# Kernel tuning notes

Measured on AMD Instinct MI355X. Metric: run time of the kernel, lower is better.

## Reference

```python
import jax, jax.numpy as jnp
import numpy as np

N_NODES = 100000
N_EDGES = 1600000
DIM = 128


def setup_inputs() -> dict:
    key = jax.random.key(0)
    k1, k2, k3, k4, k5 = jax.random.split(key, 5)
    x = jax.random.normal(k1, (N_NODES, DIM), dtype=jnp.float32)
    edge_index = jax.random.randint(k2, (2, N_EDGES), 0, N_NODES, dtype=jnp.int64)
    s = 1.0 / np.sqrt(DIM)
    W_lin = jax.random.uniform(k3, (DIM, DIM), jnp.float32, -s, s)   # nn.Linear (bias=False)
    W_gcn = jax.random.uniform(k4, (DIM, DIM), jnp.float32, -s, s)   # GCNConv internal lin (bias=False)
    b_gcn = jax.random.uniform(k5, (DIM,), jnp.float32, -s, s)       # GCNConv bias
    return {"x": x, "edge_index": edge_index, "W_lin": W_lin, "W_gcn": W_gcn, "b_gcn": b_gcn}


def reference(x, edge_index, W_lin, W_gcn, b_gcn):
    N = x.shape[0]
    # self.linear (bias=False) then GCNConv's internal linear (bias=False)
    h = (x @ W_lin.T) @ W_gcn.T                                      # [N, D]
    # add self loops (PyG GCNConv default add_self_loops=True)
    loop = jnp.arange(N, dtype=edge_index.dtype)
    row = jnp.concatenate([edge_index[0], loop])                     # source
    col = jnp.concatenate([edge_index[1], loop])                     # target
    # symmetric normalization: deg over targets incl. self loops
    deg = jax.ops.segment_sum(jnp.ones_like(col, dtype=h.dtype), col, num_segments=N)
    dinv = jnp.where(deg > 0, jax.lax.rsqrt(deg), 0.0)               # deg^{-1/2}, inf->0
    norm = dinv[row] * dinv[col]                                     # [E+N]
    # gather -> scale -> scatter-add (aggr='add', flow source_to_target)
    msg = h[row] * norm[:, None]                                     # [E+N, D]
    out = jax.ops.segment_sum(msg, col, num_segments=N) + b_gcn      # [N, D]
    # NOTE: self.relu is `Sequential as ReLU` -> empty Sequential -> identity
    return out
```

## Files before the change

kernel.cpp:

```cpp
#include <hip/hip_runtime.h>
#include <hip/hip_bf16.h>

#define DIM 128
#define NBUCK 2048
#define BCAP 1344
#define NPART 256

typedef short bf16x8 __attribute__((ext_vector_type(8)));
typedef float f32x4 __attribute__((ext_vector_type(4)));

__device__ __forceinline__ unsigned short f2bf(float f) {
    __hip_bfloat16 h = __float2bfloat16(f);
    return *reinterpret_cast<unsigned short*>(&h);
}
__device__ __forceinline__ float u2f(unsigned int u) {
    union { unsigned int i; float f; } v; v.i = u; return v.f;
}
__device__ __forceinline__ unsigned int f2u(float f) {
    union { float f; unsigned int i; } v; v.f = f; return v.i;
}

__global__ __launch_bounds__(256) void part_wp_kernel(
        const int* __restrict__ src, const int* __restrict__ dst,
        int* __restrict__ bcur, unsigned int* __restrict__ ebuf,
        int E, int nchunk,
        const float* __restrict__ Wg, const float* __restrict__ Wl,
        unsigned short* __restrict__ Wpb) {
    __shared__ int hist[NBUCK];
    __shared__ int base[NBUCK];
    const int t = threadIdx.x;

    if (blockIdx.x >= NPART) {
        const int id = (blockIdx.x - NPART) * 256 + t;
        const int c = id >> 7, k = id & 127;
        float s = 0.f;
        for (int j = 0; j < DIM; ++j)
            s = fmaf(Wg[c * DIM + j], Wl[j * DIM + k], s);
        Wpb[c * DIM + k] = f2bf(s);
        return;
    }

    for (int i = t; i < NBUCK; i += 256) hist[i] = 0;
    __syncthreads();

    const int e0 = blockIdx.x * nchunk;
    const int e1 = min(e0 + nchunk, E);
    for (int e = e0 + t; e < e1; e += 256)
        atomicAdd(&hist[dst[e] >> 6], 1);
    __syncthreads();

    for (int i = t; i < NBUCK; i += 256) {
        const int cc = hist[i];
        base[i] = (cc > 0) ? atomicAdd(&bcur[i], cc) : 0;
    }
    __syncthreads();

    for (int e = e0 + t; e < e1; e += 256) {
        const int d = dst[e];
        const int b = d >> 6;
        const int pos = atomicAdd(&base[b], 1);
        if (pos < BCAP)
            ebuf[(size_t)b * BCAP + pos] =
                (unsigned int)src[e] | ((unsigned int)(d & 63) << 17);
    }
}

__global__ __launch_bounds__(256) void gemm_bcount_kernel(
        const float* __restrict__ x, const unsigned short* __restrict__ Wpb,
        unsigned int* __restrict__ hbu,
        const unsigned int* __restrict__ ebuf, const int* __restrict__ bcur,
        int* __restrict__ degi, float* __restrict__ dinv,
        int N, int ntile) {
    __shared__ __align__(16) char smem[49152];
    const int t = threadIdx.x;

    if (blockIdx.x >= ntile) {
        int* cnt = (int*)smem;
        const int bkt = blockIdx.x - ntile;
        if (t < 64) cnt[t] = 0;
        __syncthreads();
        const int c = min(bcur[bkt], BCAP);
        const unsigned int* eb = ebuf + (size_t)bkt * BCAP;
        for (int i = t; i < c; i += 256)
            atomicAdd(&cnt[eb[i] >> 17], 1);
        __syncthreads();
        if (t < 64) {
            const int node = (bkt << 6) + t;
            if (node < N) {
                degi[node] = cnt[t];
                dinv[node] = rsqrtf((float)(cnt[t] + 1));
            }
        }
        return;
    }

    unsigned short* xs  = (unsigned short*)smem;
    unsigned short* wps = xs + 64 * 128;
    const int brow = blockIdx.x * 64;

#pragma unroll
    for (int j = 0; j < 8; ++j) {
        const int col = (t >> 4) + j * 16;
        const int kb = t & 15;
        const uint4 v = *(const uint4*)(Wpb + col * 128 + kb * 8);
        *(uint4*)&wps[col * 128 + ((kb ^ (col & 15)) * 8)] = v;
    }
#pragma unroll
    for (int i = 0; i < 4; ++i) {
        const int row = (t >> 4) + i * 16;
        const int kb = t & 15;
        const int g = brow + row;
        float4 a0 = make_float4(0.f, 0.f, 0.f, 0.f), a1 = a0;
        if (g < N) {
            a0 = *(const float4*)(x + (size_t)g * 128 + kb * 8);
            a1 = *(const float4*)(x + (size_t)g * 128 + kb * 8 + 4);
        }
        ushort4 lo, hi;
        lo.x = f2bf(a0.x); lo.y = f2bf(a0.y); lo.z = f2bf(a0.z); lo.w = f2bf(a0.w);
        hi.x = f2bf(a1.x); hi.y = f2bf(a1.y); hi.z = f2bf(a1.z); hi.w = f2bf(a1.w);
        unsigned short* p = &xs[row * 128 + ((kb ^ (row & 15)) * 8)];
        *(ushort4*)p = lo;
        *(ushort4*)(p + 4) = hi;
    }
    __syncthreads();

    const int lane = t & 63, wv = t >> 6;
    const int m16 = lane & 15, quad = lane >> 4;

    f32x4 acc[8];
#pragma unroll
    for (int ct = 0; ct < 8; ++ct) acc[ct] = (f32x4){0.f, 0.f, 0.f, 0.f};

    const int arow = wv * 16 + m16;
#pragma unroll
    for (int s = 0; s < 4; ++s) {
        const int pk = ((s * 4 + quad) ^ m16) * 8;
        const bf16x8 a = *(const bf16x8*)&xs[arow * 128 + pk];
#pragma unroll
        for (int ct = 0; ct < 8; ++ct) {
            const bf16x8 b = *(const bf16x8*)&wps[(ct * 16 + m16) * 128 + pk];
            acc[ct] = __builtin_amdgcn_mfma_f32_16x16x32_bf16(a, b, acc[ct], 0, 0, 0);
        }
    }

    const int r0 = brow + wv * 16 + quad * 4;
#pragma unroll
    for (int ct = 0; ct < 4; ++ct) {
        const int col = ct * 16 + m16;
#pragma unroll
        for (int r = 0; r < 4; ++r) {
            if (r0 + r < N) {
                const unsigned int pk = (unsigned int)f2bf(acc[ct][r]) |
                                        ((unsigned int)f2bf(acc[ct + 4][r]) << 16);
                hbu[(size_t)(r0 + r) * 64 + col] = pk;
            }
        }
    }
}

__global__ __launch_bounds__(256) void sortgather_kernel(
        const unsigned int* __restrict__ hbu, const unsigned int* __restrict__ ebuf,
        const int* __restrict__ bcur, const int* __restrict__ degi,
        const float* __restrict__ dinv,
        const float* __restrict__ b, float* __restrict__ out, int N) {
    __shared__ unsigned int pairs[BCAP * 2];
    __shared__ int cnt[64];
    __shared__ int scn[64];
    __shared__ int st[64];
    __shared__ int deg[64];
    const int t   = threadIdx.x;
    const int bkt = blockIdx.x;
    const int c   = min(bcur[bkt], BCAP);
    const unsigned int* eb = ebuf + (size_t)bkt * BCAP;
    const int n0 = bkt << 6;

    if (t < 64) {
        const int node = n0 + t;
        const int d = (node < N) ? degi[node] : 0;
        deg[t] = d;
        scn[t] = d;
    }
    __syncthreads();
    for (int off = 1; off < 64; off <<= 1) {
        int v = (t < 64 && t >= off) ? scn[t - off] : 0;
        __syncthreads();
        if (t < 64) scn[t] += v;
        __syncthreads();
    }
    if (t < 64) {
        const int excl = scn[t] - deg[t];
        st[t]  = excl;
        cnt[t] = excl;
    }
    __syncthreads();

    for (int i = t; i < c; i += 256) {
        const unsigned int p = eb[i];
        const int s = (int)(p & 0x1FFFF);
        const int pos = atomicAdd(&cnt[p >> 17], 1);
        uint2 pr; pr.x = (unsigned int)s; pr.y = f2u(dinv[s]);
        *(uint2*)&pairs[2 * pos] = pr;
    }
    __syncthreads();

    const int lane = t & 63;
    const int wv   = t >> 6;
    const float bx = b[lane];
    const float by = b[lane + 64];

    for (int i = 0; i < 16; ++i) {
        const int dl = wv * 16 + i;
        const int node = n0 + dl;
        if (node >= N) continue;
        const int dgi = deg[dl];
        const float dv = rsqrtf((float)(dgi + 1));
        const unsigned int self = hbu[(size_t)node * 64 + lane];
        float ax = dv * u2f(self << 16);
        float ay = dv * u2f(self & 0xFFFF0000u);

        const int jb = st[dl];
        const int je = jb + dgi;
        int j = jb;
        for (; j + 8 <= je; j += 8) {
            const uint2 p0 = *(const uint2*)&pairs[2 * (j + 0)];
            const uint2 p1 = *(const uint2*)&pairs[2 * (j + 1)];
            const uint2 p2 = *(const uint2*)&pairs[2 * (j + 2)];
            const uint2 p3 = *(const uint2*)&pairs[2 * (j + 3)];
            const uint2 p4 = *(const uint2*)&pairs[2 * (j + 4)];
            const uint2 p5 = *(const uint2*)&pairs[2 * (j + 5)];
            const uint2 p6 = *(const uint2*)&pairs[2 * (j + 6)];
            const uint2 p7 = *(const uint2*)&pairs[2 * (j + 7)];
            const unsigned int v0 = hbu[(size_t)p0.x * 64 + lane];
            const unsigned int v1 = hbu[(size_t)p1.x * 64 + lane];
            const unsigned int v2 = hbu[(size_t)p2.x * 64 + lane];
            const unsigned int v3 = hbu[(size_t)p3.x * 64 + lane];
            const unsigned int v4 = hbu[(size_t)p4.x * 64 + lane];
            const unsigned int v5 = hbu[(size_t)p5.x * 64 + lane];
            const unsigned int v6 = hbu[(size_t)p6.x * 64 + lane];
            const unsigned int v7 = hbu[(size_t)p7.x * 64 + lane];
            ax = fmaf(u2f(v0 << 16), u2f(p0.y), ax);
            ax = fmaf(u2f(v1 << 16), u2f(p1.y), ax);
            ax = fmaf(u2f(v2 << 16), u2f(p2.y), ax);
            ax = fmaf(u2f(v3 << 16), u2f(p3.y), ax);
            ax = fmaf(u2f(v4 << 16), u2f(p4.y), ax);
            ax = fmaf(u2f(v5 << 16), u2f(p5.y), ax);
            ax = fmaf(u2f(v6 << 16), u2f(p6.y), ax);
            ax = fmaf(u2f(v7 << 16), u2f(p7.y), ax);
            ay = fmaf(u2f(v0 & 0xFFFF0000u), u2f(p0.y), ay);
            ay = fmaf(u2f(v1 & 0xFFFF0000u), u2f(p1.y), ay);
            ay = fmaf(u2f(v2 & 0xFFFF0000u), u2f(p2.y), ay);
            ay = fmaf(u2f(v3 & 0xFFFF0000u), u2f(p3.y), ay);
            ay = fmaf(u2f(v4 & 0xFFFF0000u), u2f(p4.y), ay);
            ay = fmaf(u2f(v5 & 0xFFFF0000u), u2f(p5.y), ay);
            ay = fmaf(u2f(v6 & 0xFFFF0000u), u2f(p6.y), ay);
            ay = fmaf(u2f(v7 & 0xFFFF0000u), u2f(p7.y), ay);
        }
        for (; j + 2 <= je; j += 2) {
            const uint2 p0 = *(const uint2*)&pairs[2 * (j + 0)];
            const uint2 p1 = *(const uint2*)&pairs[2 * (j + 1)];
            const unsigned int v0 = hbu[(size_t)p0.x * 64 + lane];
            const unsigned int v1 = hbu[(size_t)p1.x * 64 + lane];
            ax = fmaf(u2f(v0 << 16), u2f(p0.y), ax);
            ax = fmaf(u2f(v1 << 16), u2f(p1.y), ax);
            ay = fmaf(u2f(v0 & 0xFFFF0000u), u2f(p0.y), ay);
            ay = fmaf(u2f(v1 & 0xFFFF0000u), u2f(p1.y), ay);
        }
        for (; j < je; ++j) {
            const uint2 pr = *(const uint2*)&pairs[2 * j];
            const unsigned int v = hbu[(size_t)pr.x * 64 + lane];
            ax = fmaf(u2f(v << 16), u2f(pr.y), ax);
            ay = fmaf(u2f(v & 0xFFFF0000u), u2f(pr.y), ay);
        }
        out[(size_t)node * 128 + lane]      = dv * ax + bx;
        out[(size_t)node * 128 + 64 + lane] = dv * ay + by;
    }
}

extern "C" void kernel_launch(void* const* d_in, const int* in_sizes, int n_in,
                              void* d_out, int out_size, void* d_ws, size_t ws_size,
                              hipStream_t stream) {
    const float* x  = (const float*)d_in[0];
    const int*   ei = (const int*)d_in[1];
    const float* Wl = (const float*)d_in[2];
    const float* Wg = (const float*)d_in[3];
    const float* bg = (const float*)d_in[4];

    const int N = in_sizes[0] / DIM;
    const int E = in_sizes[1] / 2;
    const int* srcIdx = ei;
    const int* dstIdx = ei + E;

    char* wsb = (char*)d_ws;
    unsigned short* Wpb  = (unsigned short*)(wsb + 0);
    int*            bcur = (int*)(wsb + 65536);
    int*            degi = (int*)(wsb + 131072);
    float*          dinv = (float*)(wsb + 589824);
    unsigned int*   ebuf = (unsigned int*)(wsb + 2097152);
    unsigned int*   hbu  = (unsigned int*)(wsb + 16777216);
    const size_t needed = 16777216ull + (size_t)N * DIM * 2;
    if (ws_size < needed) return;

    const int nbkt  = (N + 63) >> 6;
    const int ntile = (N + 63) >> 6;
    const int nchunk = (E + NPART - 1) / NPART;

    hipMemsetAsync(bcur, 0, NBUCK * sizeof(int), stream);
    part_wp_kernel    <<<NPART + 64, 256, 0, stream>>>(srcIdx, dstIdx, bcur, ebuf,
                                                       E, nchunk, Wg, Wl, Wpb);
    gemm_bcount_kernel<<<ntile + nbkt, 256, 0, stream>>>(x, Wpb, hbu, ebuf, bcur,
                                                         degi, dinv, N, ntile);
    sortgather_kernel <<<nbkt, 256, 0, stream>>>(hbu, ebuf, bcur, degi, dinv, bg,
                                                 (float*)d_out, N);
}
```

Baseline: 218.5 us.

## Partition edges into per-block bucket slots and split gather into half-buckets

The edge partition no longer uses global atomics to reserve bucket space. Each of 48 large blocks writes into its own fixed-capacity slot per bucket and records per-slot counts, with a global overflow list for slots that fill up. The gather kernel now runs two blocks per 64-node bucket, each taking 32 nodes, which doubles the block count and halves shared memory per block. In exchange every half-block scans the whole bucket's slots and the overflow list, so it reads the edge data twice and does more filtering work.

```diff
diff --git a/kernel.cpp b/kernel.cpp
--- a/kernel.cpp
+++ b/kernel.cpp
@@ -3,8 +3,10 @@
 
 #define DIM 128
 #define NBUCK 2048
-#define BCAP 1344
-#define NPART 256
+#define PBLK 48
+#define CAPPB 52
+#define OVFCAP 4096
+#define HCAP 896
 
 typedef short bf16x8 __attribute__((ext_vector_type(8)));
 typedef float f32x4 __attribute__((ext_vector_type(4)));
@@ -20,18 +22,17 @@
     union { float f; unsigned int i; } v; v.f = f; return v.i;
 }
 
-__global__ __launch_bounds__(256) void part_wp_kernel(
+__global__ __launch_bounds__(1024) void part_wp_kernel(
         const int* __restrict__ src, const int* __restrict__ dst,
-        int* __restrict__ bcur, unsigned int* __restrict__ ebuf,
+        unsigned int* __restrict__ ebuf, int* __restrict__ cntt,
+        int* __restrict__ ovf_cnt, uint2* __restrict__ ovf,
         int E, int nchunk,
         const float* __restrict__ Wg, const float* __restrict__ Wl,
         unsigned short* __restrict__ Wpb) {
-    __shared__ int hist[NBUCK];
-    __shared__ int base[NBUCK];
     const int t = threadIdx.x;
 
-    if (blockIdx.x >= NPART) {
-        const int id = (blockIdx.x - NPART) * 256 + t;
+    if (blockIdx.x >= PBLK) {
+        const int id = (blockIdx.x - PBLK) * 1024 + t;
         const int c = id >> 7, k = id & 127;
         float s = 0.f;
         for (int j = 0; j < DIM; ++j)
@@ -40,35 +41,41 @@
         return;
     }
 
-    for (int i = t; i < NBUCK; i += 256) hist[i] = 0;
-    __syncthreads();
-
-    const int e0 = blockIdx.x * nchunk;
+    __shared__ int hist[NBUCK];
+    const int blk = blockIdx.x;
+    for (int i = t; i < NBUCK; i += 1024) hist[i] = 0;
+    __syncthreads();
+
+    const int e0 = blk * nchunk;
     const int e1 = min(e0 + nchunk, E);
-    for (int e = e0 + t; e < e1; e += 256)
+    for (int e = e0 + t; e < e1; e += 1024)
         atomicAdd(&hist[dst[e] >> 6], 1);
     __syncthreads();
 
-    for (int i = t; i < NBUCK; i += 256) {
-        const int cc = hist[i];
-        base[i] = (cc > 0) ? atomicAdd(&bcur[i], cc) : 0;
-    }
-    __syncthreads();
-
-    for (int e = e0 + t; e < e1; e += 256) {
+    for (int i = t; i < NBUCK; i += 1024) cntt[i * PBLK + blk] = hist[i];
+    __syncthreads();
+    for (int i = t; i < NBUCK; i += 1024) hist[i] = 0;
+    __syncthreads();
+
+    for (int e = e0 + t; e < e1; e += 1024) {
         const int d = dst[e];
         const int b = d >> 6;
-        const int pos = atomicAdd(&base[b], 1);
-        if (pos < BCAP)
-            ebuf[(size_t)b * BCAP + pos] =
+        const int pos = atomicAdd(&hist[b], 1);
+        if (pos < CAPPB) {
+            ebuf[((size_t)b * PBLK + blk) * CAPPB + pos] =
                 (unsigned int)src[e] | ((unsigned int)(d & 63) << 17);
+        } else {
+            const int op = atomicAdd(ovf_cnt, 1);
+            if (op < OVFCAP) { uint2 o; o.x = (unsigned int)src[e]; o.y = (unsigned int)d; ovf[op] = o; }
+        }
     }
 }
 
 __global__ __launch_bounds__(256) void gemm_bcount_kernel(
         const float* __restrict__ x, const unsigned short* __restrict__ Wpb,
         unsigned int* __restrict__ hbu,
-        const unsigned int* __restrict__ ebuf, const int* __restrict__ bcur,
+        const unsigned int* __restrict__ ebuf, const int* __restrict__ cntt,
+        const int* __restrict__ ovf_cnt, const uint2* __restrict__ ovf,
         int* __restrict__ degi, float* __restrict__ dinv,
         int N, int ntile) {
     __shared__ __align__(16) char smem[49152];
@@ -79,10 +86,18 @@
         const int bkt = blockIdx.x - ntile;
         if (t < 64) cnt[t] = 0;
         __syncthreads();
-        const int c = min(bcur[bkt], BCAP);
-        const unsigned int* eb = ebuf + (size_t)bkt * BCAP;
-        for (int i = t; i < c; i += 256)
-            atomicAdd(&cnt[eb[i] >> 17], 1);
+        const int lane = t & 63, wv = t >> 6;
+        for (int blk = wv; blk < PBLK; blk += 4) {
+            const int c = min(cntt[bkt * PBLK + blk], CAPPB);
+            const unsigned int* eb = ebuf + ((size_t)bkt * PBLK + blk) * CAPPB;
+            for (int i = lane; i < c; i += 64)
+                atomicAdd(&cnt[eb[i] >> 17], 1);
+        }
+        const int no = min(*ovf_cnt, OVFCAP);
+        for (int i = t; i < no; i += 256) {
+            const uint2 o = ovf[i];
+            if ((int)(o.y >> 6) == bkt) atomicAdd(&cnt[o.y & 63], 1);
+        }
         __syncthreads();
         if (t < 64) {
             const int node = (bkt << 6) + t;
@@ -160,56 +175,74 @@
 
 __global__ __launch_bounds__(256) void sortgather_kernel(
         const unsigned int* __restrict__ hbu, const unsigned int* __restrict__ ebuf,
-        const int* __restrict__ bcur, const int* __restrict__ degi,
-        const float* __restrict__ dinv,
+        const int* __restrict__ cntt,
+        const int* __restrict__ ovf_cnt, const uint2* __restrict__ ovf,
+        const int* __restrict__ degi, const float* __restrict__ dinv,
         const float* __restrict__ b, float* __restrict__ out, int N) {
-    __shared__ unsigned int pairs[BCAP * 2];
-    __shared__ int cnt[64];
-    __shared__ int scn[64];
-    __shared__ int st[64];
-    __shared__ int deg[64];
+    __shared__ unsigned int pairs[HCAP * 2];
+    __shared__ int cnt[32];
+    __shared__ int scn[32];
+    __shared__ int st[32];
+    __shared__ int deg[32];
     const int t   = threadIdx.x;
-    const int bkt = blockIdx.x;
-    const int c   = min(bcur[bkt], BCAP);
-    const unsigned int* eb = ebuf + (size_t)bkt * BCAP;
-    const int n0 = bkt << 6;
-
-    if (t < 64) {
+    const int bkt = blockIdx.x >> 1;
+    const int h   = blockIdx.x & 1;
+    const int n0  = (bkt << 6) + (h << 5);
+
+    if (t < 32) {
         const int node = n0 + t;
         const int d = (node < N) ? degi[node] : 0;
         deg[t] = d;
         scn[t] = d;
     }
     __syncthreads();
-    for (int off = 1; off < 64; off <<= 1) {
-        int v = (t < 64 && t >= off) ? scn[t - off] : 0;
+    for (int off = 1; off < 32; off <<= 1) {
+        int v = (t < 32 && t >= off) ? scn[t - off] : 0;
         __syncthreads();
-        if (t < 64) scn[t] += v;
+        if (t < 32) scn[t] += v;
         __syncthreads();
     }
-    if (t < 64) {
+    if (t < 32) {
         const int excl = scn[t] - deg[t];
         st[t]  = excl;
         cnt[t] = excl;
     }
     __syncthreads();
 
-    for (int i = t; i < c; i += 256) {
-        const unsigned int p = eb[i];
-        const int s = (int)(p & 0x1FFFF);
-        const int pos = atomicAdd(&cnt[p >> 17], 1);
-        uint2 pr; pr.x = (unsigned int)s; pr.y = f2u(dinv[s]);
-        *(uint2*)&pairs[2 * pos] = pr;
-    }
-    __syncthreads();
-
-    const int lane = t & 63;
-    const int wv   = t >> 6;
+    const int lane = t & 63, wv = t >> 6;
+    for (int blk = wv; blk < PBLK; blk += 4) {
+        const int c = min(cntt[bkt * PBLK + blk], CAPPB);
+        const unsigned int* eb = ebuf + ((size_t)bkt * PBLK + blk) * CAPPB;
+        for (int i = lane; i < c; i += 64) {
+            const unsigned int p = eb[i];
+            const int dl = (int)(p >> 17);
+            if ((dl >> 5) != h) continue;
+            const int s = (int)(p & 0x1FFFF);
+            const int pos = atomicAdd(&cnt[dl & 31], 1);
+            if (pos < HCAP) {
+                uint2 pr; pr.x = (unsigned int)s; pr.y = f2u(dinv[s]);
+                *(uint2*)&pairs[2 * pos] = pr;
+            }
+        }
+    }
+    const int no = min(*ovf_cnt, OVFCAP);
+    for (int i = t; i < no; i += 256) {
+        const uint2 o = ovf[i];
+        if ((int)(o.y >> 6) != bkt) continue;
+        const int dl = (int)(o.y & 63);
+        if ((dl >> 5) != h) continue;
+        const int pos = atomicAdd(&cnt[dl & 31], 1);
+        if (pos < HCAP) {
+            uint2 pr; pr.x = o.x; pr.y = f2u(dinv[o.x]);
+            *(uint2*)&pairs[2 * pos] = pr;
+        }
+    }
+    __syncthreads();
+
     const float bx = b[lane];
     const float by = b[lane + 64];
-
-    for (int i = 0; i < 16; ++i) {
-        const int dl = wv * 16 + i;
+    for (int i = 0; i < 8; ++i) {
+        const int dl = wv * 8 + i;
         const int node = n0 + dl;
         if (node >= N) continue;
         const int dgi = deg[dl];
@@ -292,23 +325,25 @@
 
     char* wsb = (char*)d_ws;
     unsigned short* Wpb  = (unsigned short*)(wsb + 0);
-    int*            bcur = (int*)(wsb + 65536);
-    int*            degi = (int*)(wsb + 131072);
-    float*          dinv = (float*)(wsb + 589824);
+    int*            cntt = (int*)(wsb + 65536);
+    int*            ovfc = (int*)(wsb + 458752);
+    uint2*          ovf  = (uint2*)(wsb + 462848);
+    int*            degi = (int*)(wsb + 524288);
+    float*          dinv = (float*)(wsb + 983040);
     unsigned int*   ebuf = (unsigned int*)(wsb + 2097152);
-    unsigned int*   hbu  = (unsigned int*)(wsb + 16777216);
-    const size_t needed = 16777216ull + (size_t)N * DIM * 2;
+    unsigned int*   hbu  = (unsigned int*)(wsb + 22544384);
+    const size_t needed = 22544384ull + (size_t)N * DIM * 2;
     if (ws_size < needed) return;
 
     const int nbkt  = (N + 63) >> 6;
     const int ntile = (N + 63) >> 6;
-    const int nchunk = (E + NPART - 1) / NPART;
-
-    hipMemsetAsync(bcur, 0, NBUCK * sizeof(int), stream);
-    part_wp_kernel    <<<NPART + 64, 256, 0, stream>>>(srcIdx, dstIdx, bcur, ebuf,
-                                                       E, nchunk, Wg, Wl, Wpb);
-    gemm_bcount_kernel<<<ntile + nbkt, 256, 0, stream>>>(x, Wpb, hbu, ebuf, bcur,
-                                                         degi, dinv, N, ntile);
-    sortgather_kernel <<<nbkt, 256, 0, stream>>>(hbu, ebuf, bcur, degi, dinv, bg,
-                                                 (float*)d_out, N);
-}
+    const int nchunk = (E + PBLK - 1) / PBLK;
+
+    hipMemsetAsync(ovfc, 0, sizeof(int), stream);
+    part_wp_kernel    <<<PBLK + 16, 1024, 0, stream>>>(srcIdx, dstIdx, ebuf, cntt,
+                                                       ovfc, ovf, E, nchunk, Wg, Wl, Wpb);
+    gemm_bcount_kernel<<<ntile + nbkt, 256, 0, stream>>>(x, Wpb, hbu, ebuf, cntt,
+                                                         ovfc, ovf, degi, dinv, N, ntile);
+    sortgather_kernel <<<2 * nbkt, 256, 0, stream>>>(hbu, ebuf, cntt, ovfc, ovf,
+                                                     degi, dinv, bg, (float*)d_out, N);
+}
```

New measurement: 263.6 us. 20.6% more time.

## Split gather buckets into half-blocks and read pre-swizzled weights from global

Applied to the files above, without the earlier changes.

The sortgather kernel now runs two blocks per 64-node bucket, each handling 32 destination nodes and filtering the bucket's edges to its half. This doubles the grid and reduces per-block LDS so more blocks fit per CU, but each block rescans the full edge list. Separately, the GEMM kernel no longer stages the combined weight matrix in LDS. It reads B fragments directly from a pre-swizzled global copy written by the weight-product kernel, which cuts LDS from 48KB to 16KB and so allows higher occupancy, in exchange for global or L2 loads on every MFMA operand.

```diff
diff --git a/kernel.cpp b/kernel.cpp
--- a/kernel.cpp
+++ b/kernel.cpp
@@ -5,6 +5,7 @@
 #define NBUCK 2048
 #define BCAP 1344
 #define NPART 256
+#define HCAP 896
 
 typedef short bf16x8 __attribute__((ext_vector_type(8)));
 typedef float f32x4 __attribute__((ext_vector_type(4)));
@@ -25,7 +26,7 @@
         int* __restrict__ bcur, unsigned int* __restrict__ ebuf,
         int E, int nchunk,
         const float* __restrict__ Wg, const float* __restrict__ Wl,
-        unsigned short* __restrict__ Wpb) {
+        unsigned short* __restrict__ Wps) {
     __shared__ int hist[NBUCK];
     __shared__ int base[NBUCK];
     const int t = threadIdx.x;
@@ -36,7 +37,7 @@
         float s = 0.f;
         for (int j = 0; j < DIM; ++j)
             s = fmaf(Wg[c * DIM + j], Wl[j * DIM + k], s);
-        Wpb[c * DIM + k] = f2bf(s);
+        Wps[c * 128 + (((k >> 3) ^ (c & 15)) << 3) + (k & 7)] = f2bf(s);
         return;
     }
 
@@ -66,12 +67,12 @@
 }
 
 __global__ __launch_bounds__(256) void gemm_bcount_kernel(
-        const float* __restrict__ x, const unsigned short* __restrict__ Wpb,
+        const float* __restrict__ x, const unsigned short* __restrict__ Wps,
         unsigned int* __restrict__ hbu,
         const unsigned int* __restrict__ ebuf, const int* __restrict__ bcur,
         int* __restrict__ degi, float* __restrict__ dinv,
         int N, int ntile) {
-    __shared__ __align__(16) char smem[49152];
+    __shared__ __align__(16) char smem[16384];
     const int t = threadIdx.x;
 
     if (blockIdx.x >= ntile) {
@@ -94,17 +95,9 @@
         return;
     }
 
-    unsigned short* xs  = (unsigned short*)smem;
-    unsigned short* wps = xs + 64 * 128;
+    unsigned short* xs = (unsigned short*)smem;
     const int brow = blockIdx.x * 64;
 
-#pragma unroll
-    for (int j = 0; j < 8; ++j) {
-        const int col = (t >> 4) + j * 16;
-        const int kb = t & 15;
-        const uint4 v = *(const uint4*)(Wpb + col * 128 + kb * 8);
-        *(uint4*)&wps[col * 128 + ((kb ^ (col & 15)) * 8)] = v;
-    }
 #pragma unroll
     for (int i = 0; i < 4; ++i) {
         const int row = (t >> 4) + i * 16;
@@ -132,14 +125,19 @@
     for (int ct = 0; ct < 8; ++ct) acc[ct] = (f32x4){0.f, 0.f, 0.f, 0.f};
 
     const int arow = wv * 16 + m16;
+    int pk[4];
+    bf16x8 afrag[4];
 #pragma unroll
     for (int s = 0; s < 4; ++s) {
-        const int pk = ((s * 4 + quad) ^ m16) * 8;
-        const bf16x8 a = *(const bf16x8*)&xs[arow * 128 + pk];
-#pragma unroll
-        for (int ct = 0; ct < 8; ++ct) {
-            const bf16x8 b = *(const bf16x8*)&wps[(ct * 16 + m16) * 128 + pk];
-            acc[ct] = __builtin_amdgcn_mfma_f32_16x16x32_bf16(a, b, acc[ct], 0, 0, 0);
+        pk[s] = ((s * 4 + quad) ^ m16) * 8;
+        afrag[s] = *(const bf16x8*)&xs[arow * 128 + pk[s]];
+    }
+#pragma unroll
+    for (int ct = 0; ct < 8; ++ct) {
+#pragma unroll
+        for (int s = 0; s < 4; ++s) {
+            const bf16x8 b = *(const bf16x8*)&Wps[(ct * 16 + m16) * 128 + pk[s]];
+            acc[ct] = __builtin_amdgcn_mfma_f32_16x16x32_bf16(afrag[s], b, acc[ct], 0, 0, 0);
         }
     }
 
@@ -150,9 +148,9 @@
 #pragma unroll
         for (int r = 0; r < 4; ++r) {
             if (r0 + r < N) {
-                const unsigned int pk = (unsigned int)f2bf(acc[ct][r]) |
-                                        ((unsigned int)f2bf(acc[ct + 4][r]) << 16);
-                hbu[(size_t)(r0 + r) * 64 + col] = pk;
+                const unsigned int pkd = (unsigned int)f2bf(acc[ct][r]) |
+                                         ((unsigned int)f2bf(acc[ct + 4][r]) << 16);
+                hbu[(size_t)(r0 + r) * 64 + col] = pkd;
             }
         }
     }
@@ -163,31 +161,32 @@
         const int* __restrict__ bcur, const int* __restrict__ degi,
         const float* __restrict__ dinv,
         const float* __restrict__ b, float* __restrict__ out, int N) {
-    __shared__ unsigned int pairs[BCAP * 2];
-    __shared__ int cnt[64];
-    __shared__ int scn[64];
-    __shared__ int st[64];
-    __shared__ int deg[64];
+    __shared__ unsigned int pairs[HCAP * 2];
+    __shared__ int cnt[32];
+    __shared__ int scn[32];
+    __shared__ int st[32];
+    __shared__ int deg[32];
     const int t   = threadIdx.x;
-    const int bkt = blockIdx.x;
+    const int bkt = blockIdx.x >> 1;
+    const int h   = blockIdx.x & 1;
+    const int n0  = (bkt << 6) + (h << 5);
     const int c   = min(bcur[bkt], BCAP);
     const unsigned int* eb = ebuf + (size_t)bkt * BCAP;
-    const int n0 = bkt << 6;
-
-    if (t < 64) {
+
+    if (t < 32) {
         const int node = n0 + t;
         const int d = (node < N) ? degi[node] : 0;
         deg[t] = d;
         scn[t] = d;
     }
     __syncthreads();
-    for (int off = 1; off < 64; off <<= 1) {
-        int v = (t < 64 && t >= off) ? scn[t - off] : 0;
+    for (int off = 1; off < 32; off <<= 1) {
+        int v = (t < 32 && t >= off) ? scn[t - off] : 0;
         __syncthreads();
-        if (t < 64) scn[t] += v;
+        if (t < 32) scn[t] += v;
         __syncthreads();
     }
-    if (t < 64) {
+    if (t < 32) {
         const int excl = scn[t] - deg[t];
         st[t]  = excl;
         cnt[t] = excl;
@@ -196,10 +195,14 @@
 
     for (int i = t; i < c; i += 256) {
         const unsigned int p = eb[i];
+        const int dl = (int)(p >> 17);
+        if ((dl >> 5) != h) continue;
         const int s = (int)(p & 0x1FFFF);
-        const int pos = atomicAdd(&cnt[p >> 17], 1);
-        uint2 pr; pr.x = (unsigned int)s; pr.y = f2u(dinv[s]);
-        *(uint2*)&pairs[2 * pos] = pr;
+        const int pos = atomicAdd(&cnt[dl & 31], 1);
+        if (pos < HCAP) {
+            uint2 pr; pr.x = (unsigned int)s; pr.y = f2u(dinv[s]);
+            *(uint2*)&pairs[2 * pos] = pr;
+        }
     }
     __syncthreads();
 
@@ -208,8 +211,8 @@
     const float bx = b[lane];
     const float by = b[lane + 64];
 
-    for (int i = 0; i < 16; ++i) {
-        const int dl = wv * 16 + i;
+    for (int i = 0; i < 8; ++i) {
+        const int dl = wv * 8 + i;
         const int node = n0 + dl;
         if (node >= N) continue;
         const int dgi = deg[dl];
@@ -291,7 +294,7 @@
     const int* dstIdx = ei + E;
 
     char* wsb = (char*)d_ws;
-    unsigned short* Wpb  = (unsigned short*)(wsb + 0);
+    unsigned short* Wps  = (unsigned short*)(wsb + 0);
     int*            bcur = (int*)(wsb + 65536);
     int*            degi = (int*)(wsb + 131072);
     float*          dinv = (float*)(wsb + 589824);
@@ -306,9 +309,9 @@
 
     hipMemsetAsync(bcur, 0, NBUCK * sizeof(int), stream);
     part_wp_kernel    <<<NPART + 64, 256, 0, stream>>>(srcIdx, dstIdx, bcur, ebuf,
-                                                       E, nchunk, Wg, Wl, Wpb);
-    gemm_bcount_kernel<<<ntile + nbkt, 256, 0, stream>>>(x, Wpb, hbu, ebuf, bcur,
+                                                       E, nchunk, Wg, Wl, Wps);
+    gemm_bcount_kernel<<<ntile + nbkt, 256, 0, stream>>>(x, Wps, hbu, ebuf, bcur,
                                                          degi, dinv, N, ntile);
-    sortgather_kernel <<<nbkt, 256, 0, stream>>>(hbu, ebuf, bcur, degi, dinv, bg,
-                                                 (float*)d_out, N);
-}
+    sortgather_kernel <<<2 * nbkt, 256, 0, stream>>>(hbu, ebuf, bcur, degi, dinv, bg,
+                                                     (float*)d_out, N);
+}
```

Result: no change. 220.6 us (+0.9%).
